# Performance work log

Hardware: AMD Instinct MI355X
Metric: run time of the kernel (lower is better)

The kernel has to match this reference:

```python
import jax, jax.numpy as jnp
import numpy as np

VOCAB, EMBED, HIDDEN = 32000, 512, 1024
B, S = 16, 128

def setup_inputs() -> dict:
    key = jax.random.key(0)
    ks = jax.random.split(key, 10)
    sc = lambda fan: 1.0 / np.sqrt(fan)
    return {
        "tgt": jax.random.randint(ks[0], (B, S), 0, VOCAB),
        "h": jax.random.normal(ks[1], (B, HIDDEN), jnp.float32),
        "c": jax.random.normal(ks[2], (B, HIDDEN), jnp.float32),
        "emb": jax.random.normal(ks[3], (VOCAB, EMBED), jnp.float32),
        "W_ih": jax.random.uniform(ks[4], (4 * HIDDEN, EMBED), jnp.float32, -sc(HIDDEN), sc(HIDDEN)),
        "W_hh": jax.random.uniform(ks[5], (4 * HIDDEN, HIDDEN), jnp.float32, -sc(HIDDEN), sc(HIDDEN)),
        "b_ih": jax.random.uniform(ks[6], (4 * HIDDEN,), jnp.float32, -sc(HIDDEN), sc(HIDDEN)),
        "b_hh": jax.random.uniform(ks[7], (4 * HIDDEN,), jnp.float32, -sc(HIDDEN), sc(HIDDEN)),
        "W_fc": jax.random.uniform(ks[8], (VOCAB, HIDDEN), jnp.float32, -sc(HIDDEN), sc(HIDDEN)),
        "b_fc": jax.random.uniform(ks[9], (VOCAB,), jnp.float32, -sc(HIDDEN), sc(HIDDEN)),
    }

def reference(tgt, h, c, emb, W_ih, W_hh, b_ih, b_hh, W_fc, b_fc):
    # Embedding lookup for all steps at once; dropout is identity (eval mode).
    x = emb[tgt]  # [B,S,E]
    # Precompute input-to-gate projections for every timestep (parallel part).
    xg = jnp.einsum('bse,ge->bsg', x, W_ih) + b_ih + b_hh  # [B,S,4H]

    Hn = h.shape[-1]

    def step(carry, xg_t):
        h, c = carry
        gates = xg_t + h @ W_hh.T  # [B,4H]
        i, f, g, o = jnp.split(gates, 4, axis=-1)
        i = jax.nn.sigmoid(i)
        f = jax.nn.sigmoid(f)
        g = jnp.tanh(g)
        o = jax.nn.sigmoid(o)
        c = f * c + i * g
        h = o * jnp.tanh(c)
        return (h, c), h

    (_, _), hs = jax.lax.scan(step, (h, c), jnp.swapaxes(xg, 0, 1))  # hs: [S,B,H]
    hs = jnp.swapaxes(hs, 0, 1)  # [B,S,H]
    logits = jnp.einsum('bsh,vh->bsv', hs, W_fc) + b_fc  # [B,S,V]
    return logits
```

## Files before the change

### kernel.cpp

```cpp
#include <hip/hip_runtime.h>

typedef unsigned short u16;
typedef unsigned int   u32;
typedef unsigned long long u64;
typedef __attribute__((ext_vector_type(8))) short short8;
typedef __attribute__((ext_vector_type(4))) float f32x4;

#define B_   16
#define S_   128
#define H_   1024
#define E_   512
#define V_   32000

static __device__ __forceinline__ float bf2f(u16 x){
  u32 u = ((u32)x) << 16; float f; __builtin_memcpy(&f, &u, 4); return f;
}
static __device__ __forceinline__ u16 f2bf(float f){
  u32 u; __builtin_memcpy(&u, &f, 4);
  u += 0x7fffu + ((u >> 16) & 1u);
  return (u16)(u >> 16);
}
static __device__ __forceinline__ void gl2lds16(const void* g, void* l){
  __builtin_amdgcn_global_load_lds((const __attribute__((address_space(1))) u32*)g,
                                   (__attribute__((address_space(3))) u32*)l, 16, 0, 0);
}
static __device__ __forceinline__ float sigm(float x){ return 1.0f/(1.0f + __expf(-x)); }
static __device__ __forceinline__ float tanh_f(float x){
  float a = fabsf(x);
  float e = __expf(-2.0f*a);
  float r = (1.0f - e)/(1.0f + e);
  return x < 0.0f ? -r : r;
}
static __device__ __forceinline__ float ldf(const void* base, long i, int is32){
  return is32 ? ((const float*)base)[i] : bf2f(((const u16*)base)[i]);
}
static __device__ __forceinline__ short8 load8(const void* base, long i, int is32){
  short8 r;
  if (is32){
    const float* p = (const float*)base + i;
    f32x4 a = *(const f32x4*)p;
    f32x4 b = *(const f32x4*)(p + 4);
    r[0]=(short)f2bf(a[0]); r[1]=(short)f2bf(a[1]);
    r[2]=(short)f2bf(a[2]); r[3]=(short)f2bf(a[3]);
    r[4]=(short)f2bf(b[0]); r[5]=(short)f2bf(b[1]);
    r[6]=(short)f2bf(b[2]); r[7]=(short)f2bf(b[3]);
  } else {
    r = *(const short8*)((const u16*)base + i);
  }
  return r;
}

static __device__ __forceinline__ short8 ld_frag_dev(const u16* p){
  u64 a = __hip_atomic_load((const u64*)p,       __ATOMIC_RELAXED, __HIP_MEMORY_SCOPE_AGENT);
  u64 b = __hip_atomic_load((const u64*)(p + 4), __ATOMIC_RELAXED, __HIP_MEMORY_SCOPE_AGENT);
  short8 r;
  __builtin_memcpy(&r, &a, 8);
  __builtin_memcpy((char*)&r + 8, &b, 8);
  return r;
}
static __device__ __forceinline__ void st_dev_u16(u16* p, u16 v){
  __hip_atomic_store(p, v, __ATOMIC_RELAXED, __HIP_MEMORY_SCOPE_AGENT);
}

#define SPIN_CAP 1048576u

__global__ void k_detect(const u32* __restrict__ h32, u32* __restrict__ flag,
                         u32* __restrict__ arr, u32* __restrict__ bar_gen){
  const int lane = threadIdx.x;
  int cnt = 0;
  for (int i = 0; i < 16; ++i){
    u32 w = h32[lane*16 + i];
    u32 e = (w >> 7) & 0xFFu;
    cnt += (e >= 100u && e <= 140u) ? 1 : 0;
  }
  __hip_atomic_store(arr + lane*32, 0u, __ATOMIC_RELAXED, __HIP_MEMORY_SCOPE_AGENT);
  for (int off = 32; off; off >>= 1) cnt += __shfl_down(cnt, off, 64);
  if (lane == 0){
    flag[0] = (cnt < 512) ? 1u : 0u;
    __hip_atomic_store(bar_gen, 0u, __ATOMIC_RELAXED, __HIP_MEMORY_SCOPE_AGENT);
  }
}

__global__ __launch_bounds__(256) void k_wfc(const void* __restrict__ W_fc,
                                             u16* __restrict__ out,
                                             const u32* __restrict__ flag){
  if (!flag[0]) return;
  const long total = (long)V_*H_;
  long i = ((long)blockIdx.x*256 + threadIdx.x)*8;
  const long stride = (long)gridDim.x*256*8;
  for (; i < total; i += stride)
    *(short8*)(out + i) = load8(W_fc, i, 1);
}

__global__ __launch_bounds__(256) void k_xg(
    const int* __restrict__ tgt, const void* __restrict__ emb,
    const void* __restrict__ W_ih, const void* __restrict__ b_ih,
    const void* __restrict__ b_hh, float* __restrict__ xg,
    const u32* __restrict__ flag)
{
  const int is32 = (int)flag[0];
  __shared__ __align__(16) u16 la[64*32];
  __shared__ __align__(16) u16 lb[64*32];
  __shared__ int ids[64];
  const int nb = blockIdx.x;
  const int mb = blockIdx.y;
  const int tid = threadIdx.x, lane = tid & 63, wv = tid >> 6;
  const int wm = wv >> 1, wn = wv & 1;
  const int g0 = nb*64;

  if (tid < 64){
    int m = mb*64 + tid;
    ids[tid] = tgt[(m & 15)*S_ + (m >> 4)];
  }
  __syncthreads();

  f32x4 acc[2][2];
#pragma unroll
  for (int i = 0; i < 2; ++i)
#pragma unroll
    for (int j = 0; j < 2; ++j) acc[i][j] = (f32x4){0.f,0.f,0.f,0.f};

  const int srow = tid >> 2, sk = (tid & 3)*8;
  const long arow = (long)ids[srow]*E_ + sk;
  const long brow = (long)(g0 + srow)*E_ + sk;

  for (int k0 = 0; k0 < E_; k0 += 32){
    short8 va = load8(emb,  arow + k0, is32);
    short8 vb = load8(W_ih, brow + k0, is32);
    *(short8*)&la[srow*32 + sk] = va;
    *(short8*)&lb[srow*32 + sk] = vb;
    __syncthreads();
    short8 af[2], bfv[2];
#pragma unroll
    for (int mt = 0; mt < 2; ++mt)
      af[mt] = *(const short8*)&la[(wm*32 + mt*16 + (lane & 15))*32 + ((lane >> 4)*8)];
#pragma unroll
    for (int nt = 0; nt < 2; ++nt)
      bfv[nt] = *(const short8*)&lb[(wn*32 + nt*16 + (lane & 15))*32 + ((lane >> 4)*8)];
#pragma unroll
    for (int mt = 0; mt < 2; ++mt)
#pragma unroll
      for (int nt = 0; nt < 2; ++nt)
        acc[mt][nt] = __builtin_amdgcn_mfma_f32_16x16x32_bf16(af[mt], bfv[nt], acc[mt][nt], 0,0,0);
    __syncthreads();
  }

  const int col = lane & 15, quad = lane >> 4;
#pragma unroll
  for (int nt = 0; nt < 2; ++nt){
    int g = g0 + wn*32 + nt*16 + col;
    float bias = ldf(b_ih, g, is32) + ldf(b_hh, g, is32);
    int q = g >> 10, r = g & 1023;
#pragma unroll
    for (int mt = 0; mt < 2; ++mt){
      int t = mb*4 + wm*2 + mt;
      f32x4 v;
      v[0] = acc[mt][nt][0] + bias;
      v[1] = acc[mt][nt][1] + bias;
      v[2] = acc[mt][nt][2] + bias;
      v[3] = acc[mt][nt][3] + bias;
      *(f32x4*)(xg + ((long)((t*4 + q)*1024 + r)*16 + quad*4)) = v;
    }
  }
}

__global__ __launch_bounds__(256, 1) void k_steps_all(
    const void* __restrict__ W_hh, const float* __restrict__ xg,
    const void* __restrict__ h_in, const void* __restrict__ c_in,
    u16* __restrict__ h_buf, u16* __restrict__ hs,
    const u32* __restrict__ flag, u32* arr, u32* bar_gen)
{
  const int is32 = (int)flag[0];
  const int s    = blockIdx.x;
  const int tid  = threadIdx.x;
  const int lane = tid & 63;
  const int wv   = tid >> 6;

  __shared__ __align__(16) float part[4][4][16][20];

  short8 wf[4][8];
#pragma unroll
  for (int q = 0; q < 4; ++q){
    const long wrow = (long)(q*H_ + s*16 + (lane & 15))*H_ + wv*256 + ((lane >> 4)*8);
#pragma unroll
    for (int j = 0; j < 8; ++j)
      wf[q][j] = load8(W_hh, wrow + j*32, is32);
  }

  const int eb = tid >> 4;
  const int er = tid & 15;
  const int co = eb*H_ + s*16 + er;
  float c_val = ldf(c_in, co, is32);

  const int arow = (lane & 15)*H_ + wv*256 + ((lane >> 4)*8);
  const float* xg_b = xg + (s*16 + er)*16 + eb;
  u16* hs_b = hs + (long)eb*S_*H_ + s*16 + er;

  {
    float hv0 = ldf(h_in, co, is32);
    u16 hi0 = f2bf(hv0);
    st_dev_u16(h_buf + co,         hi0);
    st_dev_u16(h_buf + B_*H_ + co, f2bf(hv0 - bf2f(hi0)));
  }
  __syncthreads();
  if (tid == 0)
    __hip_atomic_store(arr + s*32, 1u, __ATOMIC_RELAXED, __HIP_MEMORY_SCOPE_AGENT);

  for (int t = 0; t < S_; ++t){
    const float* xg_t = xg_b + (long)t*65536;
    float pre0 = xg_t[0], pre1 = xg_t[16384], pre2 = xg_t[32768], pre3 = xg_t[49152];

    const u32 tgen = (u32)(t + 1);
    if (s == 0 && tid < 64){
      u32 iters = 0;
      while (true){
        u32 v = __hip_atomic_load(arr + tid*32, __ATOMIC_RELAXED, __HIP_MEMORY_SCOPE_AGENT);
        if (__all((int)(v >= tgen))) break;
        if (++iters > SPIN_CAP) break;
        __builtin_amdgcn_s_sleep(1);
      }
      if (tid == 0)
        __hip_atomic_store(bar_gen, tgen, __ATOMIC_RELAXED, __HIP_MEMORY_SCOPE_AGENT);
    } else if (tid == 0){
      u32 iters = 0;
      while (__hip_atomic_load(bar_gen, __ATOMIC_RELAXED, __HIP_MEMORY_SCOPE_AGENT) < tgen){
        if (++iters > SPIN_CAP) break;
        __builtin_amdgcn_s_sleep(1);
      }
    }
    __syncthreads();

    const u16* hp = h_buf + (t & 1)*(2*B_*H_) + arow;
    short8 ahi[8], alo[8];
#pragma unroll
    for (int j = 0; j < 8; ++j){
      ahi[j] = ld_frag_dev(hp + j*32);
      alo[j] = ld_frag_dev(hp + B_*H_ + j*32);
    }

    f32x4 acc[4];
#pragma unroll
    for (int q = 0; q < 4; ++q) acc[q] = (f32x4){0.f,0.f,0.f,0.f};
#pragma unroll
    for (int j = 0; j < 8; ++j){
#pragma unroll
      for (int q = 0; q < 4; ++q){
        acc[q] = __builtin_amdgcn_mfma_f32_16x16x32_bf16(ahi[j], wf[q][j], acc[q], 0,0,0);
        acc[q] = __builtin_amdgcn_mfma_f32_16x16x32_bf16(alo[j], wf[q][j], acc[q], 0,0,0);
      }
    }
#pragma unroll
    for (int q = 0; q < 4; ++q)
      *(f32x4*)&part[wv][q][lane & 15][(lane >> 4)*4] = acc[q];
    __syncthreads();

    float p0 = pre0, p1 = pre1, p2 = pre2, p3 = pre3;
#pragma unroll
    for (int w = 0; w < 4; ++w){
      p0 += part[w][0][er][eb];
      p1 += part[w][1][er][eb];
      p2 += part[w][2][er][eb];
      p3 += part[w][3][er][eb];
    }
    float iv = sigm(p0), fv = sigm(p1), gv = tanh_f(p2), ov = sigm(p3);
    c_val = fv*c_val + iv*gv;
    float hv = ov*tanh_f(c_val);
    u16 hi = f2bf(hv);
    u16 lo = f2bf(hv - bf2f(hi));
    const int po = ((t + 1) & 1)*(2*B_*H_);
    st_dev_u16(h_buf + po + co,         hi);
    st_dev_u16(h_buf + po + B_*H_ + co, lo);

    __syncthreads();
    if (tid == 0)
      __hip_atomic_store(arr + s*32, (u32)(t + 2), __ATOMIC_RELAXED, __HIP_MEMORY_SCOPE_AGENT);
    hs_b[(long)t*H_] = hi;
  }
}

__global__ __launch_bounds__(256) void k_logits(
    const u16* __restrict__ hs, const void* __restrict__ W_fc,
    const u16* __restrict__ wcvt, const void* __restrict__ b_fc,
    void* __restrict__ outv, const u32* __restrict__ flag)
{
  const int is32 = (int)flag[0];
  __shared__ __align__(16) u16 la[128*32];
  __shared__ __align__(16) u16 lb[128*32];
  const int lin  = blockIdx.x;
  const int lin2 = (lin & 7)*500 + (lin >> 3);
  const int mb = lin2 & 15;
  const int nb = lin2 >> 4;
  const int tid = threadIdx.x, lane = tid & 63, wv = tid >> 6;
  const int wm = wv >> 1, wn = wv & 1;
  const long m0 = (long)mb*128;
  const long n0 = (long)nb*128;

  const u16* Wb = is32 ? wcvt : (const u16*)W_fc;

  f32x4 acc[4][4];
#pragma unroll
  for (int i = 0; i < 4; ++i)
#pragma unroll
    for (int j = 0; j < 4; ++j) acc[i][j] = (f32x4){0.f,0.f,0.f,0.f};

  const int srow = lane >> 2, scol = (lane & 3)*8;
  const u16* asrc = hs + (m0 + wv*32 + srow)*H_ + scol;
  u16* lda = &la[wv*32*32];
  const u16* bsrc = Wb ? Wb + (n0 + wv*32 + srow)*H_ + scol : (const u16*)0;
  u16* ldb = &lb[wv*32*32];
  const int br = tid >> 2, bk = (tid & 3)*8;
  const long brow0 = (long)(n0 + br)*H_ + bk;
  const long brow1 = (long)(n0 + br + 64)*H_ + bk;

  for (int k0 = 0; k0 < H_; k0 += 32){
    gl2lds16(asrc + k0,          lda);
    gl2lds16(asrc + 16*H_ + k0,  lda + 16*32);
    if (Wb){
      gl2lds16(bsrc + k0,          ldb);
      gl2lds16(bsrc + 16*H_ + k0,  ldb + 16*32);
    } else {
      *(short8*)&lb[br*32 + bk]        = load8(W_fc, brow0 + k0, 1);
      *(short8*)&lb[(br + 64)*32 + bk] = load8(W_fc, brow1 + k0, 1);
    }
    __syncthreads();
    short8 af[4], bfr[4];
#pragma unroll
    for (int mt = 0; mt < 4; ++mt)
      af[mt] = *(const short8*)&la[(wm*64 + mt*16 + (lane & 15))*32 + ((lane >> 4)*8)];
#pragma unroll
    for (int nt = 0; nt < 4; ++nt)
      bfr[nt] = *(const short8*)&lb[(wn*64 + nt*16 + (lane & 15))*32 + ((lane >> 4)*8)];
#pragma unroll
    for (int mt = 0; mt < 4; ++mt)
#pragma unroll
      for (int nt = 0; nt < 4; ++nt)
        acc[mt][nt] = __builtin_amdgcn_mfma_f32_16x16x32_bf16(af[mt], bfr[nt], acc[mt][nt], 0,0,0);
    __syncthreads();
  }

  const int col = lane & 15, quad = lane >> 4;
#pragma unroll
  for (int nt = 0; nt < 4; ++nt){
    long n = n0 + wn*64 + nt*16 + col;
    float bias = ldf(b_fc, n, is32);
#pragma unroll
    for (int mt = 0; mt < 4; ++mt){
      long m = m0 + wm*64 + mt*16 + quad*4;
      float v0 = acc[mt][nt][0] + bias;
      float v1 = acc[mt][nt][1] + bias;
      float v2 = acc[mt][nt][2] + bias;
      float v3 = acc[mt][nt][3] + bias;
      if (is32){
        float* p = (float*)outv + m*V_ + n;
        __builtin_nontemporal_store(v0, p);
        __builtin_nontemporal_store(v1, p + V_);
        __builtin_nontemporal_store(v2, p + 2L*V_);
        __builtin_nontemporal_store(v3, p + 3L*V_);
      } else {
        u16* p = (u16*)outv + m*V_ + n;
        __builtin_nontemporal_store(f2bf(v0), p);
        __builtin_nontemporal_store(f2bf(v1), p + V_);
        __builtin_nontemporal_store(f2bf(v2), p + 2L*V_);
        __builtin_nontemporal_store(f2bf(v3), p + 3L*V_);
      }
    }
  }
}

extern "C" void kernel_launch(void* const* d_in, const int* in_sizes, int n_in,
                              void* d_out, int out_size, void* d_ws, size_t ws_size,
                              hipStream_t stream)
{
  (void)in_sizes; (void)n_in; (void)out_size;
  const int*  tgt  = (const int*)d_in[0];
  const void* h0   = d_in[1];
  const void* c0   = d_in[2];
  const void* emb  = d_in[3];
  const void* W_ih = d_in[4];
  const void* W_hh = d_in[5];
  const void* b_ih = d_in[6];
  const void* b_hh = d_in[7];
  const void* W_fc = d_in[8];
  const void* b_fc = d_in[9];

  float* xg = (float*)d_out;
  char* ws    = (char*)d_ws;
  u16*   hs      = (u16*)(ws);
  u16*   h_buf   = (u16*)(ws + 4194304);
  u32*   flag    = (u32*)(ws + 4325376);
  u32*   arr     = (u32*)(ws + 4325504);
  u32*   bar_gen = (u32*)(ws + 4333696);
  u16*   wcvt  = (ws_size >= (size_t)4334080 + 65536000u) ? (u16*)(ws + 4334080)
                                                          : (u16*)0;

  k_detect<<<1, 64, 0, stream>>>((const u32*)h0, flag, arr, bar_gen);
  dim3 gA(64, 32);
  k_xg<<<gA, 256, 0, stream>>>(tgt, emb, W_ih, b_ih, b_hh, xg, flag);
  if (wcvt)
    k_wfc<<<2048, 256, 0, stream>>>(W_fc, wcvt, flag);

  u16* hb  = h_buf;
  u16* hsp = hs;
  void* args[9];
  args[0] = (void*)&W_hh;
  args[1] = (void*)&xg;
  args[2] = (void*)&h0;
  args[3] = (void*)&c0;
  args[4] = (void*)&hb;
  args[5] = (void*)&hsp;
  args[6] = (void*)&flag;
  args[7] = (void*)&arr;
  args[8] = (void*)&bar_gen;
  hipLaunchCooperativeKernel((const void*)k_steps_all, dim3(64), dim3(256),
                             args, 0, stream);

  dim3 gC(4000);
  k_logits<<<gC, 256, 0, stream>>>(hs, W_fc, wcvt, b_fc, d_out, flag);
}
```

Measured before the change: 1.367 ms.

## Fuse LSTM recurrence with logits GEMM via persistent cooperative kernel and ticket queue

Adds a persistent cooperative kernel with 256 blocks. The first 64 blocks run the LSTM recurrence while the others, and later all blocks, pull logits tiles from an atomic ticket counter. Each tile waits on a progress counter until its group of 8 timesteps has been produced, so the output projection overlaps the serial recurrence instead of running afterward. It also reorders the logits tiles by timestep groups and moves xg to workspace so it does not alias the output. The fused path only runs when the workspace is large enough, otherwise the old three-kernel path is used. Risks include spin-wait contention hurting the latency-critical recurrence blocks and a co-residency requirement for 256 blocks.

```diff
diff --git a/kernel.cpp b/kernel.cpp
--- a/kernel.cpp
+++ b/kernel.cpp
@@ -61,11 +61,18 @@
 static __device__ __forceinline__ void st_dev_u16(u16* p, u16 v){
   __hip_atomic_store(p, v, __ATOMIC_RELAXED, __HIP_MEMORY_SCOPE_AGENT);
 }
+static __device__ __forceinline__ u32 ld_dev_u32(const u32* p){
+  return __hip_atomic_load(p, __ATOMIC_RELAXED, __HIP_MEMORY_SCOPE_AGENT);
+}
+static __device__ __forceinline__ void st_dev_u32(u32* p, u32 v){
+  __hip_atomic_store(p, v, __ATOMIC_RELAXED, __HIP_MEMORY_SCOPE_AGENT);
+}
 
 #define SPIN_CAP 1048576u
 
 __global__ void k_detect(const u32* __restrict__ h32, u32* __restrict__ flag,
-                         u32* __restrict__ arr, u32* __restrict__ bar_gen){
+                         u32* __restrict__ arr, u32* __restrict__ bar_gen,
+                         u32* __restrict__ prog, u32* __restrict__ ticket){
   const int lane = threadIdx.x;
   int cnt = 0;
   for (int i = 0; i < 16; ++i){
@@ -73,11 +80,13 @@
     u32 e = (w >> 7) & 0xFFu;
     cnt += (e >= 100u && e <= 140u) ? 1 : 0;
   }
-  __hip_atomic_store(arr + lane*32, 0u, __ATOMIC_RELAXED, __HIP_MEMORY_SCOPE_AGENT);
+  st_dev_u32(arr + lane*32, 0u);
   for (int off = 32; off; off >>= 1) cnt += __shfl_down(cnt, off, 64);
   if (lane == 0){
     flag[0] = (cnt < 512) ? 1u : 0u;
-    __hip_atomic_store(bar_gen, 0u, __ATOMIC_RELAXED, __HIP_MEMORY_SCOPE_AGENT);
+    st_dev_u32(bar_gen, 0u);
+    st_dev_u32(prog, 0u);
+    st_dev_u32(ticket, 0u);
   }
 }
 
@@ -164,138 +173,14 @@
   }
 }
 
-__global__ __launch_bounds__(256, 1) void k_steps_all(
-    const void* __restrict__ W_hh, const float* __restrict__ xg,
-    const void* __restrict__ h_in, const void* __restrict__ c_in,
-    u16* __restrict__ h_buf, u16* __restrict__ hs,
-    const u32* __restrict__ flag, u32* arr, u32* bar_gen)
+static __device__ __forceinline__ void logits_tile(
+    const u16* __restrict__ hs, const u16* Wb, const void* __restrict__ W_fc,
+    const void* __restrict__ b_fc, void* __restrict__ outv,
+    int is32, int jt, int np, int tid, u16* la, u16* lb)
 {
-  const int is32 = (int)flag[0];
-  const int s    = blockIdx.x;
-  const int tid  = threadIdx.x;
-  const int lane = tid & 63;
-  const int wv   = tid >> 6;
-
-  __shared__ __align__(16) float part[4][4][16][20];
-
-  short8 wf[4][8];
-#pragma unroll
-  for (int q = 0; q < 4; ++q){
-    const long wrow = (long)(q*H_ + s*16 + (lane & 15))*H_ + wv*256 + ((lane >> 4)*8);
-#pragma unroll
-    for (int j = 0; j < 8; ++j)
-      wf[q][j] = load8(W_hh, wrow + j*32, is32);
-  }
-
-  const int eb = tid >> 4;
-  const int er = tid & 15;
-  const int co = eb*H_ + s*16 + er;
-  float c_val = ldf(c_in, co, is32);
-
-  const int arow = (lane & 15)*H_ + wv*256 + ((lane >> 4)*8);
-  const float* xg_b = xg + (s*16 + er)*16 + eb;
-  u16* hs_b = hs + (long)eb*S_*H_ + s*16 + er;
-
-  {
-    float hv0 = ldf(h_in, co, is32);
-    u16 hi0 = f2bf(hv0);
-    st_dev_u16(h_buf + co,         hi0);
-    st_dev_u16(h_buf + B_*H_ + co, f2bf(hv0 - bf2f(hi0)));
-  }
-  __syncthreads();
-  if (tid == 0)
-    __hip_atomic_store(arr + s*32, 1u, __ATOMIC_RELAXED, __HIP_MEMORY_SCOPE_AGENT);
-
-  for (int t = 0; t < S_; ++t){
-    const float* xg_t = xg_b + (long)t*65536;
-    float pre0 = xg_t[0], pre1 = xg_t[16384], pre2 = xg_t[32768], pre3 = xg_t[49152];
-
-    const u32 tgen = (u32)(t + 1);
-    if (s == 0 && tid < 64){
-      u32 iters = 0;
-      while (true){
-        u32 v = __hip_atomic_load(arr + tid*32, __ATOMIC_RELAXED, __HIP_MEMORY_SCOPE_AGENT);
-        if (__all((int)(v >= tgen))) break;
-        if (++iters > SPIN_CAP) break;
-        __builtin_amdgcn_s_sleep(1);
-      }
-      if (tid == 0)
-        __hip_atomic_store(bar_gen, tgen, __ATOMIC_RELAXED, __HIP_MEMORY_SCOPE_AGENT);
-    } else if (tid == 0){
-      u32 iters = 0;
-      while (__hip_atomic_load(bar_gen, __ATOMIC_RELAXED, __HIP_MEMORY_SCOPE_AGENT) < tgen){
-        if (++iters > SPIN_CAP) break;
-        __builtin_amdgcn_s_sleep(1);
-      }
-    }
-    __syncthreads();
-
-    const u16* hp = h_buf + (t & 1)*(2*B_*H_) + arow;
-    short8 ahi[8], alo[8];
-#pragma unroll
-    for (int j = 0; j < 8; ++j){
-      ahi[j] = ld_frag_dev(hp + j*32);
-      alo[j] = ld_frag_dev(hp + B_*H_ + j*32);
-    }
-
-    f32x4 acc[4];
-#pragma unroll
-    for (int q = 0; q < 4; ++q) acc[q] = (f32x4){0.f,0.f,0.f,0.f};
-#pragma unroll
-    for (int j = 0; j < 8; ++j){
-#pragma unroll
-      for (int q = 0; q < 4; ++q){
-        acc[q] = __builtin_amdgcn_mfma_f32_16x16x32_bf16(ahi[j], wf[q][j], acc[q], 0,0,0);
-        acc[q] = __builtin_amdgcn_mfma_f32_16x16x32_bf16(alo[j], wf[q][j], acc[q], 0,0,0);
-      }
-    }
-#pragma unroll
-    for (int q = 0; q < 4; ++q)
-      *(f32x4*)&part[wv][q][lane & 15][(lane >> 4)*4] = acc[q];
-    __syncthreads();
-
-    float p0 = pre0, p1 = pre1, p2 = pre2, p3 = pre3;
-#pragma unroll
-    for (int w = 0; w < 4; ++w){
-      p0 += part[w][0][er][eb];
-      p1 += part[w][1][er][eb];
-      p2 += part[w][2][er][eb];
-      p3 += part[w][3][er][eb];
-    }
-    float iv = sigm(p0), fv = sigm(p1), gv = tanh_f(p2), ov = sigm(p3);
-    c_val = fv*c_val + iv*gv;
-    float hv = ov*tanh_f(c_val);
-    u16 hi = f2bf(hv);
-    u16 lo = f2bf(hv - bf2f(hi));
-    const int po = ((t + 1) & 1)*(2*B_*H_);
-    st_dev_u16(h_buf + po + co,         hi);
-    st_dev_u16(h_buf + po + B_*H_ + co, lo);
-
-    __syncthreads();
-    if (tid == 0)
-      __hip_atomic_store(arr + s*32, (u32)(t + 2), __ATOMIC_RELAXED, __HIP_MEMORY_SCOPE_AGENT);
-    hs_b[(long)t*H_] = hi;
-  }
-}
-
-__global__ __launch_bounds__(256) void k_logits(
-    const u16* __restrict__ hs, const void* __restrict__ W_fc,
-    const u16* __restrict__ wcvt, const void* __restrict__ b_fc,
-    void* __restrict__ outv, const u32* __restrict__ flag)
-{
-  const int is32 = (int)flag[0];
-  __shared__ __align__(16) u16 la[128*32];
-  __shared__ __align__(16) u16 lb[128*32];
-  const int lin  = blockIdx.x;
-  const int lin2 = (lin & 7)*500 + (lin >> 3);
-  const int mb = lin2 & 15;
-  const int nb = lin2 >> 4;
-  const int tid = threadIdx.x, lane = tid & 63, wv = tid >> 6;
+  const int lane = tid & 63, wv = tid >> 6;
   const int wm = wv >> 1, wn = wv & 1;
-  const long m0 = (long)mb*128;
-  const long n0 = (long)nb*128;
-
-  const u16* Wb = is32 ? wcvt : (const u16*)W_fc;
+  const long n0 = (long)np*128;
 
   f32x4 acc[4][4];
 #pragma unroll
@@ -304,7 +189,9 @@
     for (int j = 0; j < 4; ++j) acc[i][j] = (f32x4){0.f,0.f,0.f,0.f};
 
   const int srow = lane >> 2, scol = (lane & 3)*8;
-  const u16* asrc = hs + (m0 + wv*32 + srow)*H_ + scol;
+  const int r0 = wv*32 + srow, r1 = r0 + 16;
+  const long arow0 = ((long)(r0 >> 3)*S_ + jt*8 + (r0 & 7))*H_ + scol;
+  const long arow1 = ((long)(r1 >> 3)*S_ + jt*8 + (r1 & 7))*H_ + scol;
   u16* lda = &la[wv*32*32];
   const u16* bsrc = Wb ? Wb + (n0 + wv*32 + srow)*H_ + scol : (const u16*)0;
   u16* ldb = &lb[wv*32*32];
@@ -313,11 +200,11 @@
   const long brow1 = (long)(n0 + br + 64)*H_ + bk;
 
   for (int k0 = 0; k0 < H_; k0 += 32){
-    gl2lds16(asrc + k0,          lda);
-    gl2lds16(asrc + 16*H_ + k0,  lda + 16*32);
+    gl2lds16(hs + arow0 + k0, lda);
+    gl2lds16(hs + arow1 + k0, lda + 16*32);
     if (Wb){
-      gl2lds16(bsrc + k0,          ldb);
-      gl2lds16(bsrc + 16*H_ + k0,  ldb + 16*32);
+      gl2lds16(bsrc + k0,         ldb);
+      gl2lds16(bsrc + 16*H_ + k0, ldb + 16*32);
     } else {
       *(short8*)&lb[br*32 + bk]        = load8(W_fc, brow0 + k0, 1);
       *(short8*)&lb[(br + 64)*32 + bk] = load8(W_fc, brow1 + k0, 1);
@@ -345,7 +232,8 @@
     float bias = ldf(b_fc, n, is32);
 #pragma unroll
     for (int mt = 0; mt < 4; ++mt){
-      long m = m0 + wm*64 + mt*16 + quad*4;
+      int tr0 = wm*64 + mt*16 + quad*4;
+      long m = (long)(tr0 >> 3)*S_ + jt*8 + (tr0 & 7);
       float v0 = acc[mt][nt][0] + bias;
       float v1 = acc[mt][nt][1] + bias;
       float v2 = acc[mt][nt][2] + bias;
@@ -367,6 +255,294 @@
   }
 }
 
+__global__ __launch_bounds__(256, 1) void k_steps_all(
+    const void* __restrict__ W_hh, const float* __restrict__ xg,
+    const void* __restrict__ h_in, const void* __restrict__ c_in,
+    u16* __restrict__ h_buf, u16* __restrict__ hs,
+    const u32* __restrict__ flag, u32* arr, u32* bar_gen)
+{
+  const int is32 = (int)flag[0];
+  const int s    = blockIdx.x;
+  const int tid  = threadIdx.x;
+  const int lane = tid & 63;
+  const int wv   = tid >> 6;
+
+  __shared__ __align__(16) float part[4][4][16][20];
+
+  short8 wf[4][8];
+#pragma unroll
+  for (int q = 0; q < 4; ++q){
+    const long wrow = (long)(q*H_ + s*16 + (lane & 15))*H_ + wv*256 + ((lane >> 4)*8);
+#pragma unroll
+    for (int j = 0; j < 8; ++j)
+      wf[q][j] = load8(W_hh, wrow + j*32, is32);
+  }
+
+  const int eb = tid >> 4;
+  const int er = tid & 15;
+  const int co = eb*H_ + s*16 + er;
+  float c_val = ldf(c_in, co, is32);
+
+  const int arow = (lane & 15)*H_ + wv*256 + ((lane >> 4)*8);
+  const float* xg_b = xg + (s*16 + er)*16 + eb;
+  u16* hs_b = hs + (long)eb*S_*H_ + s*16 + er;
+
+  {
+    float hv0 = ldf(h_in, co, is32);
+    u16 hi0 = f2bf(hv0);
+    st_dev_u16(h_buf + co,         hi0);
+    st_dev_u16(h_buf + B_*H_ + co, f2bf(hv0 - bf2f(hi0)));
+  }
+  __syncthreads();
+  if (tid == 0) st_dev_u32(arr + s*32, 1u);
+
+  for (int t = 0; t < S_; ++t){
+    const float* xg_t = xg_b + (long)t*65536;
+    float pre0 = xg_t[0], pre1 = xg_t[16384], pre2 = xg_t[32768], pre3 = xg_t[49152];
+
+    const u32 tgen = (u32)(t + 1);
+    if (s == 0 && tid < 64){
+      u32 iters = 0;
+      while (true){
+        u32 v = ld_dev_u32(arr + tid*32);
+        if (__all((int)(v >= tgen))) break;
+        if (++iters > SPIN_CAP) break;
+        __builtin_amdgcn_s_sleep(1);
+      }
+      if (tid == 0) st_dev_u32(bar_gen, tgen);
+    } else if (tid == 0){
+      u32 iters = 0;
+      while (ld_dev_u32(bar_gen) < tgen){
+        if (++iters > SPIN_CAP) break;
+        __builtin_amdgcn_s_sleep(1);
+      }
+    }
+    __syncthreads();
+
+    const u16* hp = h_buf + (t & 1)*(2*B_*H_) + arow;
+    short8 ahi[8], alo[8];
+#pragma unroll
+    for (int j = 0; j < 8; ++j){
+      ahi[j] = ld_frag_dev(hp + j*32);
+      alo[j] = ld_frag_dev(hp + B_*H_ + j*32);
+    }
+
+    f32x4 acc[4];
+#pragma unroll
+    for (int q = 0; q < 4; ++q) acc[q] = (f32x4){0.f,0.f,0.f,0.f};
+#pragma unroll
+    for (int j = 0; j < 8; ++j){
+#pragma unroll
+      for (int q = 0; q < 4; ++q){
+        acc[q] = __builtin_amdgcn_mfma_f32_16x16x32_bf16(ahi[j], wf[q][j], acc[q], 0,0,0);
+        acc[q] = __builtin_amdgcn_mfma_f32_16x16x32_bf16(alo[j], wf[q][j], acc[q], 0,0,0);
+      }
+    }
+#pragma unroll
+    for (int q = 0; q < 4; ++q)
+      *(f32x4*)&part[wv][q][lane & 15][(lane >> 4)*4] = acc[q];
+    __syncthreads();
+
+    float p0 = pre0, p1 = pre1, p2 = pre2, p3 = pre3;
+#pragma unroll
+    for (int w = 0; w < 4; ++w){
+      p0 += part[w][0][er][eb];
+      p1 += part[w][1][er][eb];
+      p2 += part[w][2][er][eb];
+      p3 += part[w][3][er][eb];
+    }
+    float iv = sigm(p0), fv = sigm(p1), gv = tanh_f(p2), ov = sigm(p3);
+    c_val = fv*c_val + iv*gv;
+    float hv = ov*tanh_f(c_val);
+    u16 hi = f2bf(hv);
+    u16 lo = f2bf(hv - bf2f(hi));
+    const int po = ((t + 1) & 1)*(2*B_*H_);
+    st_dev_u16(h_buf + po + co,         hi);
+    st_dev_u16(h_buf + po + B_*H_ + co, lo);
+
+    __syncthreads();
+    if (tid == 0) st_dev_u32(arr + s*32, (u32)(t + 2));
+    hs_b[(long)t*H_] = hi;
+  }
+}
+
+__global__ __launch_bounds__(256) void k_logits(
+    const u16* __restrict__ hs, const void* __restrict__ W_fc,
+    const u16* __restrict__ wcvt, const void* __restrict__ b_fc,
+    void* __restrict__ outv, const u32* __restrict__ flag)
+{
+  const int is32 = (int)flag[0];
+  __shared__ __align__(16) u16 la[128*32];
+  __shared__ __align__(16) u16 lb[128*32];
+  const int lin  = blockIdx.x;
+  const int lin2 = (lin & 7)*500 + (lin >> 3);
+  const int jt = lin2 & 15;
+  const int np = lin2 >> 4;
+  const u16* Wb = is32 ? wcvt : (const u16*)W_fc;
+  logits_tile(hs, Wb, W_fc, b_fc, outv, is32, jt, np, (int)threadIdx.x, la, lb);
+}
+
+__global__ __launch_bounds__(256, 1) void k_fused(
+    const void* __restrict__ W_hh, const float* __restrict__ xg,
+    const void* __restrict__ h_in, const void* __restrict__ c_in,
+    u16* __restrict__ h_buf, u16* __restrict__ hs,
+    const u32* __restrict__ flag, u32* arr, u32* bar_gen, u32* prog,
+    u32* ticket, const void* __restrict__ W_fc, const u16* __restrict__ wcvt,
+    const void* __restrict__ b_fc, void* __restrict__ outv)
+{
+  const int is32 = (int)flag[0];
+  const int s    = blockIdx.x;
+  const int tid  = threadIdx.x;
+
+  __shared__ __align__(16) float part[4][4][16][20];
+  __shared__ __align__(16) u16 la[128*32];
+  __shared__ __align__(16) u16 lb[128*32];
+  __shared__ int tks;
+
+  if (s < 64){
+    const int lane = tid & 63;
+    const int wv   = tid >> 6;
+
+    short8 wf[4][8];
+#pragma unroll
+    for (int q = 0; q < 4; ++q){
+      const long wrow = (long)(q*H_ + s*16 + (lane & 15))*H_ + wv*256 + ((lane >> 4)*8);
+#pragma unroll
+      for (int j = 0; j < 8; ++j)
+        wf[q][j] = load8(W_hh, wrow + j*32, is32);
+    }
+
+    const int eb = tid >> 4;
+    const int er = tid & 15;
+    const int co = eb*H_ + s*16 + er;
+    float c_val = ldf(c_in, co, is32);
+
+    const int arow = (lane & 15)*H_ + wv*256 + ((lane >> 4)*8);
+    const float* xg_b = xg + (s*16 + er)*16 + eb;
+    u16* hs_b = hs + (long)eb*S_*H_ + s*16 + er;
+
+    {
+      float hv0 = ldf(h_in, co, is32);
+      u16 hi0 = f2bf(hv0);
+      st_dev_u16(h_buf + co,         hi0);
+      st_dev_u16(h_buf + B_*H_ + co, f2bf(hv0 - bf2f(hi0)));
+    }
+    __syncthreads();
+    if (tid == 0) st_dev_u32(arr + s*32, 1u);
+
+    for (int t = 0; t < S_; ++t){
+      const float* xg_t = xg_b + (long)t*65536;
+      float pre0 = xg_t[0], pre1 = xg_t[16384], pre2 = xg_t[32768], pre3 = xg_t[49152];
+
+      const u32 tgen = (u32)(t + 1);
+      if (s == 0 && tid < 64){
+        u32 iters = 0;
+        while (true){
+          u32 v = ld_dev_u32(arr + tid*32);
+          if (__all((int)(v >= tgen))) break;
+          if (++iters > SPIN_CAP) break;
+          __builtin_amdgcn_s_sleep(1);
+        }
+        if (tid == 0){
+          st_dev_u32(bar_gen, tgen);
+          st_dev_u32(prog, tgen);
+        }
+      } else if (tid == 0){
+        u32 iters = 0;
+        while (ld_dev_u32(bar_gen) < tgen){
+          if (++iters > SPIN_CAP) break;
+          __builtin_amdgcn_s_sleep(1);
+        }
+      }
+      __syncthreads();
+
+      const u16* hp = h_buf + (t & 1)*(2*B_*H_) + arow;
+      short8 ahi[8], alo[8];
+#pragma unroll
+      for (int j = 0; j < 8; ++j){
+        ahi[j] = ld_frag_dev(hp + j*32);
+        alo[j] = ld_frag_dev(hp + B_*H_ + j*32);
+      }
+
+      f32x4 acc[4];
+#pragma unroll
+      for (int q = 0; q < 4; ++q) acc[q] = (f32x4){0.f,0.f,0.f,0.f};
+#pragma unroll
+      for (int j = 0; j < 8; ++j){
+#pragma unroll
+        for (int q = 0; q < 4; ++q){
+          acc[q] = __builtin_amdgcn_mfma_f32_16x16x32_bf16(ahi[j], wf[q][j], acc[q], 0,0,0);
+          acc[q] = __builtin_amdgcn_mfma_f32_16x16x32_bf16(alo[j], wf[q][j], acc[q], 0,0,0);
+        }
+      }
+#pragma unroll
+      for (int q = 0; q < 4; ++q)
+        *(f32x4*)&part[wv][q][lane & 15][(lane >> 4)*4] = acc[q];
+      __syncthreads();
+
+      float p0 = pre0, p1 = pre1, p2 = pre2, p3 = pre3;
+#pragma unroll
+      for (int w = 0; w < 4; ++w){
+        p0 += part[w][0][er][eb];
+        p1 += part[w][1][er][eb];
+        p2 += part[w][2][er][eb];
+        p3 += part[w][3][er][eb];
+      }
+      float iv = sigm(p0), fv = sigm(p1), gv = tanh_f(p2), ov = sigm(p3);
+      c_val = fv*c_val + iv*gv;
+      float hv = ov*tanh_f(c_val);
+      u16 hi = f2bf(hv);
+      u16 lo = f2bf(hv - bf2f(hi));
+      const int po = ((t + 1) & 1)*(2*B_*H_);
+      st_dev_u16(h_buf + po + co,         hi);
+      st_dev_u16(h_buf + po + B_*H_ + co, lo);
+      st_dev_u16(hs_b + (long)t*H_, hi);
+
+      __syncthreads();
+      if (tid == 0) st_dev_u32(arr + s*32, (u32)(t + 2));
+    }
+
+    if (s == 0){
+      if (tid < 64){
+        u32 iters = 0;
+        while (true){
+          u32 v = ld_dev_u32(arr + tid*32);
+          if (__all((int)(v >= (u32)(S_ + 1)))) break;
+          if (++iters > SPIN_CAP) break;
+          __builtin_amdgcn_s_sleep(1);
+        }
+      }
+      __syncthreads();
+      if (tid == 0){
+        st_dev_u32(bar_gen, (u32)(S_ + 1));
+        st_dev_u32(prog,    (u32)(S_ + 1));
+      }
+    }
+  }
+
+  const u16* Wb = is32 ? wcvt : (const u16*)W_fc;
+  for (;;){
+    __syncthreads();
+    if (tid == 0)
+      tks = (int)__hip_atomic_fetch_add(ticket, 1u, __ATOMIC_RELAXED, __HIP_MEMORY_SCOPE_AGENT);
+    __syncthreads();
+    const int tile = tks;
+    if (tile >= 16*250) break;
+    const int jt = tile / 250;
+    const int np = tile - jt*250;
+    if (tid == 0){
+      const u32 need = (u32)(jt*8 + 9);
+      u32 iters = 0;
+      while (ld_dev_u32(prog) < need){
+        if (++iters > SPIN_CAP) break;
+        __builtin_amdgcn_s_sleep(32);
+      }
+    }
+    __syncthreads();
+    logits_tile(hs, Wb, W_fc, b_fc, outv, is32, jt, np, tid, la, lb);
+  }
+}
+
 extern "C" void kernel_launch(void* const* d_in, const int* in_sizes, int n_in,
                               void* d_out, int out_size, void* d_ws, size_t ws_size,
                               hipStream_t stream)
@@ -383,37 +559,54 @@
   const void* W_fc = d_in[8];
   const void* b_fc = d_in[9];
 
-  float* xg = (float*)d_out;
-  char* ws    = (char*)d_ws;
+  char* ws = (char*)d_ws;
   u16*   hs      = (u16*)(ws);
   u16*   h_buf   = (u16*)(ws + 4194304);
   u32*   flag    = (u32*)(ws + 4325376);
   u32*   arr     = (u32*)(ws + 4325504);
   u32*   bar_gen = (u32*)(ws + 4333696);
-  u16*   wcvt  = (ws_size >= (size_t)4334080 + 65536000u) ? (u16*)(ws + 4334080)
-                                                          : (u16*)0;
-
-  k_detect<<<1, 64, 0, stream>>>((const u32*)h0, flag, arr, bar_gen);
-  dim3 gA(64, 32);
-  k_xg<<<gA, 256, 0, stream>>>(tgt, emb, W_ih, b_ih, b_hh, xg, flag);
-  if (wcvt)
+  u32*   prog    = (u32*)(ws + 4333824);
+  u32*   ticket  = (u32*)(ws + 4333952);
+  const size_t WCVT_OFF = 4334080;
+  const size_t XG_OFF   = WCVT_OFF + 65536000u;
+  const size_t NEED_FB  = WCVT_OFF + 65536000u;
+  const size_t NEED_OV  = XG_OFF   + 33554432u;
+
+  u16* wcvt = (ws_size >= NEED_FB) ? (u16*)(ws + WCVT_OFF) : (u16*)0;
+  const int overlap = (ws_size >= NEED_OV);
+
+  k_detect<<<1, 64, 0, stream>>>((const u32*)h0, flag, arr, bar_gen, prog, ticket);
+
+  if (overlap){
+    float* xg = (float*)(ws + XG_OFF);
+    dim3 gA(64, 32);
+    k_xg<<<gA, 256, 0, stream>>>(tgt, emb, W_ih, b_ih, b_hh, xg, flag);
     k_wfc<<<2048, 256, 0, stream>>>(W_fc, wcvt, flag);
 
-  u16* hb  = h_buf;
-  u16* hsp = hs;
-  void* args[9];
-  args[0] = (void*)&W_hh;
-  args[1] = (void*)&xg;
-  args[2] = (void*)&h0;
-  args[3] = (void*)&c0;
-  args[4] = (void*)&hb;
-  args[5] = (void*)&hsp;
-  args[6] = (void*)&flag;
-  args[7] = (void*)&arr;
-  args[8] = (void*)&bar_gen;
-  hipLaunchCooperativeKernel((const void*)k_steps_all, dim3(64), dim3(256),
-                             args, 0, stream);
-
-  dim3 gC(4000);
-  k_logits<<<gC, 256, 0, stream>>>(hs, W_fc, wcvt, b_fc, d_out, flag);
-}
+    void* args[15];
+    u16* hb = h_buf;  u16* hsp = hs;
+    args[0]  = (void*)&W_hh;  args[1]  = (void*)&xg;     args[2]  = (void*)&h0;
+    args[3]  = (void*)&c0;    args[4]  = (void*)&hb;     args[5]  = (void*)&hsp;
+    args[6]  = (void*)&flag;  args[7]  = (void*)&arr;    args[8]  = (void*)&bar_gen;
+    args[9]  = (void*)&prog;  args[10] = (void*)&ticket; args[11] = (void*)&W_fc;
+    args[12] = (void*)&wcvt;  args[13] = (void*)&b_fc;   args[14] = (void*)&d_out;
+    hipLaunchCooperativeKernel((const void*)k_fused, dim3(256), dim3(256),
+                               args, 0, stream);
+  } else {
+    float* xg = (float*)d_out;
+    dim3 gA(64, 32);
+    k_xg<<<gA, 256, 0, stream>>>(tgt, emb, W_ih, b_ih, b_hh, xg, flag);
+    if (wcvt) k_wfc<<<2048, 256, 0, stream>>>(W_fc, wcvt, flag);
+
+    u16* hb = h_buf;  u16* hsp = hs;
+    void* args[9];
+    args[0] = (void*)&W_hh; args[1] = (void*)&xg;   args[2] = (void*)&h0;
+    args[3] = (void*)&c0;   args[4] = (void*)&hb;   args[5] = (void*)&hsp;
+    args[6] = (void*)&flag; args[7] = (void*)&arr;  args[8] = (void*)&bar_gen;
+    hipLaunchCooperativeKernel((const void*)k_steps_all, dim3(64), dim3(256),
+                               args, 0, stream);
+
+    dim3 gC(4000);
+    k_logits<<<gC, 256, 0, stream>>>(hs, W_fc, wcvt, b_fc, d_out, flag);
+  }
+}
```

Result: faster. 1.216 ms (-11.0%).
